# Performance work log

Hardware: AMD Instinct MI355X
Metric: run time of the kernel (lower is better)

The kernel has to match this reference:

```python
import jax, jax.numpy as jnp
import numpy as np

FH, FW = 3, 3          # kernel_size
SHIFT = 0.1            # input_shift


def extract_patches(x, fh, fw):
    # x: [B, C, H, W] -> patches flattened in (fh, fw, C) order: [B, fh*fw*C, Ho, Wo]
    B, C, H, W = x.shape
    Ho, Wo = H - fh + 1, W - fw + 1
    slices = [x[:, :, i:i + Ho, j:j + Wo] for i in range(fh) for j in range(fw)]
    p = jnp.stack(slices, axis=1)            # [B, fh*fw, C, Ho, Wo]
    return p.reshape(B, fh * fw * C, Ho, Wo)


def setup_inputs() -> dict:
    key = jax.random.key(0)
    kx, kk1, kk2 = jax.random.split(key, 3)
    B, C, H, W, O = 8, 32, 32, 32, 64
    x = jax.random.normal(kx, (B, C, H, W), dtype=jnp.float32)
    # xavier-uniform-style init for kernels (fh, fw, C, O)
    lim = float(np.sqrt(6.0 / (FH * FW * C + FH * FW * O)))
    k1 = jax.random.uniform(kk1, (FH, FW, C, O), minval=-lim, maxval=lim, dtype=jnp.float32)
    k2 = jax.random.uniform(kk2, (FH, FW, C, O), minval=-lim, maxval=lim, dtype=jnp.float32)
    bias = jnp.zeros((O,), dtype=jnp.float32)
    return {"x": x, "k1": k1, "k2": k2, "bias": bias}


def _branch(logp, kflat):
    # logp: [B, P, Ho, Wo], kflat: [P, O] -> max-plus over P, then exp: [B, O, Ho, Wo]
    return jnp.exp(jnp.max(logp[:, :, None, :, :] + kflat[None, :, :, None, None], axis=1))


def reference(x, k1, k2, bias):
    O = k1.shape[-1]
    k1f = k1.reshape(-1, O)   # (fh*fw*C, O) matches patch flatten order
    k2f = k2.reshape(-1, O)
    logp_pos = jnp.log(jnp.maximum(extract_patches(x, FH, FW), SHIFT))
    logp_neg = jnp.log(jnp.maximum(extract_patches(-x, FH, FW), SHIFT))
    y11 = _branch(logp_pos, k1f)
    y12 = _branch(logp_pos, k2f)
    y21 = _branch(logp_neg, k1f)
    y22 = _branch(logp_neg, k2f)
    return y11 - y12 - y21 + y22 + bias[None, :, None, None]
```

## Files before the change

### kernel.cpp

```cpp
#include <hip/hip_runtime.h>

namespace {

constexpr int FHc = 3, FWc = 3;
constexpr int Bc = 8, Cc = 32, Hc = 32, Wc = 32, Oc = 64;
constexpr int HOc = 30, WOc = 30;
constexpr float SHIFTc = 0.1f;
constexpr int SW = 4;
constexpr int RW = SW + FWc - 1;
constexpr int ROWW = 8;
constexpr int TILE_F = Cc * FHc * ROWW;

#define LOADROW6(dst, base) do {                                        \
    const float4 _a = *reinterpret_cast<const float4*>(base);           \
    const float2 _b = *reinterpret_cast<const float2*>((base) + 4);     \
    dst[0]=_a.x; dst[1]=_a.y; dst[2]=_a.z; dst[3]=_a.w;                 \
    dst[4]=_b.x; dst[5]=_b.y; } while (0)

__global__ __launch_bounds__(256, 4)
void bipolar_morph2d(const float* __restrict__ x,
                     const float* __restrict__ k1,
                     const float* __restrict__ k2,
                     const float* __restrict__ bias,
                     float* __restrict__ out)
{
    __shared__ float sh[4096];
    float* lp = sh;
    float* ln = sh + TILE_F;

    const int tid = threadIdx.x;
    const int bid = blockIdx.x;
    const int wt  = bid & 7;
    const int ho  = (bid >> 3) % HOc;
    const int b   = bid / (8 * HOc);
    const int wo0 = wt * SW;

    for (int e = tid; e < Cc * FHc * RW; e += 256) {
        const int c   = e / (FHc * RW);
        const int rem = e - c * (FHc * RW);
        const int i   = rem / RW;
        const int w   = rem - i * RW;
        int col = wo0 + w; if (col > Wc - 1) col = Wc - 1;
        const float xv = x[((b * Cc + c) * Hc + (ho + i)) * Wc + col];
        lp[(c * FHc + i) * ROWW + w] = __logf(fmaxf(xv,  SHIFTc));
        ln[(c * FHc + i) * ROWW + w] = __logf(fmaxf(-xv, SHIFTc));
    }
    __syncthreads();

    const int wv    = tid >> 6;
    const int o     = tid & 63;
    const int cbase = wv * 8;

    float m11[SW], m12[SW], m21[SW], m22[SW];
    #pragma unroll
    for (int s = 0; s < SW; ++s) m11[s] = m12[s] = m21[s] = m22[s] = -1e30f;

    #pragma unroll 1
    for (int c = cbase; c < cbase + 8; ++c) {
        #pragma unroll
        for (int i = 0; i < FHc; ++i) {
            const int p0 = (i * FWc * Cc + c) * Oc + o;
            const float k1j0 = k1[p0], k1j1 = k1[p0 + Cc * Oc], k1j2 = k1[p0 + 2 * Cc * Oc];
            const float k2j0 = k2[p0], k2j1 = k2[p0 + Cc * Oc], k2j2 = k2[p0 + 2 * Cc * Oc];

            float r[RW];
            LOADROW6(r, &lp[(c * FHc + i) * ROWW]);
            #pragma unroll
            for (int s = 0; s < SW; ++s) {
                m11[s] = fmaxf(m11[s], fmaxf(fmaxf(r[s] + k1j0, r[s + 1] + k1j1), r[s + 2] + k1j2));
                m12[s] = fmaxf(m12[s], fmaxf(fmaxf(r[s] + k2j0, r[s + 1] + k2j1), r[s + 2] + k2j2));
            }
            LOADROW6(r, &ln[(c * FHc + i) * ROWW]);
            #pragma unroll
            for (int s = 0; s < SW; ++s) {
                m21[s] = fmaxf(m21[s], fmaxf(fmaxf(r[s] + k1j0, r[s + 1] + k1j1), r[s + 2] + k1j2));
                m22[s] = fmaxf(m22[s], fmaxf(fmaxf(r[s] + k2j0, r[s + 1] + k2j1), r[s + 2] + k2j2));
            }
        }
    }

    __syncthreads();
    #pragma unroll
    for (int s = 0; s < SW; ++s) {
        sh[((wv * 4 + 0) * SW + s) * 64 + o] = m11[s];
        sh[((wv * 4 + 1) * SW + s) * 64 + o] = m12[s];
        sh[((wv * 4 + 2) * SW + s) * 64 + o] = m21[s];
        sh[((wv * 4 + 3) * SW + s) * 64 + o] = m22[s];
    }
    __syncthreads();

    const int s  = wv;
    const int wo = wo0 + s;
    if (wo < WOc) {
        const float bo = bias[o];
        float f[4];
        #pragma unroll
        for (int br = 0; br < 4; ++br) {
            const float v0 = sh[((0 * 4 + br) * SW + s) * 64 + o];
            const float v1 = sh[((1 * 4 + br) * SW + s) * 64 + o];
            const float v2 = sh[((2 * 4 + br) * SW + s) * 64 + o];
            const float v3 = sh[((3 * 4 + br) * SW + s) * 64 + o];
            f[br] = fmaxf(fmaxf(v0, v1), fmaxf(v2, v3));
        }
        out[((b * Oc + o) * HOc + ho) * WOc + wo] =
            __expf(f[0]) - __expf(f[1]) - __expf(f[2]) + __expf(f[3]) + bo;
    }
}

}

extern "C" void kernel_launch(void* const* d_in, const int* in_sizes, int n_in,
                              void* d_out, int out_size, void* d_ws, size_t ws_size,
                              hipStream_t stream) {
    const float* x    = (const float*)d_in[0];
    const float* k1   = (const float*)d_in[1];
    const float* k2   = (const float*)d_in[2];
    const float* bias = (const float*)d_in[3];
    float* out        = (float*)d_out;

    const int nblocks = Bc * HOc * 8;
    bipolar_morph2d<<<dim3(nblocks), dim3(256), 0, stream>>>(x, k1, k2, bias, out);
}
```

Measured before the change: 31.67 us.

## Precompute log-transformed input in prep kernel and read rows from global memory

Adds a prep kernel that computes log(max(±x, shift)) once for the whole input and interleaves k1/k2 into float2 pairs in the workspace. The main kernel then drops the per-block shared-memory staging and its barrier, and loads input rows straight from global/cache memory. Each loop iteration now handles two channels, which gives more independent max-plus work per step. The cost is a second kernel launch, a workspace round-trip, and reliance on cache hits for the repeated row loads.

Result: slower. 36.86 us (+16.4%).

```diff
diff --git a/kernel.cpp b/kernel.cpp
--- a/kernel.cpp
+++ b/kernel.cpp
@@ -7,26 +7,43 @@
 constexpr int HOc = 30, WOc = 30;
 constexpr float SHIFTc = 0.1f;
 constexpr int SW = 4;
-constexpr int RW = SW + FWc - 1;
-constexpr int ROWW = 8;
-constexpr int TILE_F = Cc * FHc * ROWW;
+constexpr int NX = Bc * Cc * Hc * Wc;
+constexpr int NK = FHc * FWc * Cc * Oc;
+constexpr int LN_OFF = NX;
+constexpr int KT_OFF = 2 * NX;
 
-#define LOADROW6(dst, base) do {                                        \
-    const float4 _a = *reinterpret_cast<const float4*>(base);           \
-    const float2 _b = *reinterpret_cast<const float2*>((base) + 4);     \
-    dst[0]=_a.x; dst[1]=_a.y; dst[2]=_a.z; dst[3]=_a.w;                 \
+__global__ __launch_bounds__(256)
+void prep_kernel(const float* __restrict__ x, const float* __restrict__ k1,
+                 const float* __restrict__ k2, float* __restrict__ ws)
+{
+    const int bid = blockIdx.x;
+    if (bid < NX / 256) {
+        const int t = bid * 256 + threadIdx.x;
+        const float xv = x[t];
+        ws[t]          = __logf(fmaxf(xv,  SHIFTc));
+        ws[LN_OFF + t] = __logf(fmaxf(-xv, SHIFTc));
+    } else {
+        const int t = (bid - NX / 256) * 256 + threadIdx.x;
+        if (t < NK) {
+            float2* kt = reinterpret_cast<float2*>(ws + KT_OFF);
+            kt[t] = make_float2(k1[t], k2[t]);
+        }
+    }
+}
+
+#define LDROW6(dst, p) do {                                              \
+    const float4 _a = *reinterpret_cast<const float4*>(p);               \
+    const float2 _b = *reinterpret_cast<const float2*>((p) + 4);         \
+    dst[0]=_a.x; dst[1]=_a.y; dst[2]=_a.z; dst[3]=_a.w;                  \
     dst[4]=_b.x; dst[5]=_b.y; } while (0)
 
+#define M3(m, a, b) (m) = fmaxf(fmaxf((m), (a)), (b))
+
 __global__ __launch_bounds__(256, 4)
-void bipolar_morph2d(const float* __restrict__ x,
-                     const float* __restrict__ k1,
-                     const float* __restrict__ k2,
-                     const float* __restrict__ bias,
-                     float* __restrict__ out)
+void bipolar_main(const float* __restrict__ ws, const float* __restrict__ bias,
+                  float* __restrict__ out)
 {
     __shared__ float sh[4096];
-    float* lp = sh;
-    float* ln = sh + TILE_F;
 
     const int tid = threadIdx.x;
     const int bid = blockIdx.x;
@@ -34,52 +51,54 @@
     const int ho  = (bid >> 3) % HOc;
     const int b   = bid / (8 * HOc);
     const int wo0 = wt * SW;
+    const int o   = tid & 63;
+    const int wv  = __builtin_amdgcn_readfirstlane(tid >> 6);
+    const int cbase = wv * 8;
 
-    for (int e = tid; e < Cc * FHc * RW; e += 256) {
-        const int c   = e / (FHc * RW);
-        const int rem = e - c * (FHc * RW);
-        const int i   = rem / RW;
-        const int w   = rem - i * RW;
-        int col = wo0 + w; if (col > Wc - 1) col = Wc - 1;
-        const float xv = x[((b * Cc + c) * Hc + (ho + i)) * Wc + col];
-        lp[(c * FHc + i) * ROWW + w] = __logf(fmaxf(xv,  SHIFTc));
-        ln[(c * FHc + i) * ROWW + w] = __logf(fmaxf(-xv, SHIFTc));
-    }
-    __syncthreads();
-
-    const int wv    = tid >> 6;
-    const int o     = tid & 63;
-    const int cbase = wv * 8;
+    const float2* __restrict__ kt = reinterpret_cast<const float2*>(ws + KT_OFF);
 
     float m11[SW], m12[SW], m21[SW], m22[SW];
     #pragma unroll
     for (int s = 0; s < SW; ++s) m11[s] = m12[s] = m21[s] = m22[s] = -1e30f;
 
     #pragma unroll 1
-    for (int c = cbase; c < cbase + 8; ++c) {
+    for (int cp = 0; cp < 4; ++cp) {
+        const int c0 = cbase + cp * 2;
         #pragma unroll
         for (int i = 0; i < FHc; ++i) {
-            const int p0 = (i * FWc * Cc + c) * Oc + o;
-            const float k1j0 = k1[p0], k1j1 = k1[p0 + Cc * Oc], k1j2 = k1[p0 + 2 * Cc * Oc];
-            const float k2j0 = k2[p0], k2j1 = k2[p0 + Cc * Oc], k2j2 = k2[p0 + 2 * Cc * Oc];
+            const float* lp0 = ws + ((b * Cc + c0) * Hc + (ho + i)) * Wc + wo0;
+            float rlp0[6], rlp1[6], rln0[6], rln1[6];
+            LDROW6(rlp0, lp0);
+            LDROW6(rlp1, lp0 + Hc * Wc);
+            LDROW6(rln0, lp0 + LN_OFF);
+            LDROW6(rln1, lp0 + LN_OFF + Hc * Wc);
 
-            float r[RW];
-            LOADROW6(r, &lp[(c * FHc + i) * ROWW]);
+            const int kb = (i * FWc * Cc + c0) * Oc + o;
+            const float2 ka0 = kt[kb],                 kb0 = kt[kb + Oc];
+            const float2 ka1 = kt[kb + Cc * Oc],       kb1 = kt[kb + Cc * Oc + Oc];
+            const float2 ka2 = kt[kb + 2 * Cc * Oc],   kb2 = kt[kb + 2 * Cc * Oc + Oc];
+
             #pragma unroll
             for (int s = 0; s < SW; ++s) {
-                m11[s] = fmaxf(m11[s], fmaxf(fmaxf(r[s] + k1j0, r[s + 1] + k1j1), r[s + 2] + k1j2));
-                m12[s] = fmaxf(m12[s], fmaxf(fmaxf(r[s] + k2j0, r[s + 1] + k2j1), r[s + 2] + k2j2));
-            }
-            LOADROW6(r, &ln[(c * FHc + i) * ROWW]);
-            #pragma unroll
-            for (int s = 0; s < SW; ++s) {
-                m21[s] = fmaxf(m21[s], fmaxf(fmaxf(r[s] + k1j0, r[s + 1] + k1j1), r[s + 2] + k1j2));
-                m22[s] = fmaxf(m22[s], fmaxf(fmaxf(r[s] + k2j0, r[s + 1] + k2j1), r[s + 2] + k2j2));
+                M3(m11[s], rlp0[s] + ka0.x, rlp0[s+1] + ka1.x);
+                M3(m11[s], rlp0[s+2] + ka2.x, rlp1[s] + kb0.x);
+                M3(m11[s], rlp1[s+1] + kb1.x, rlp1[s+2] + kb2.x);
+
+                M3(m12[s], rlp0[s] + ka0.y, rlp0[s+1] + ka1.y);
+                M3(m12[s], rlp0[s+2] + ka2.y, rlp1[s] + kb0.y);
+                M3(m12[s], rlp1[s+1] + kb1.y, rlp1[s+2] + kb2.y);
+
+                M3(m21[s], rln0[s] + ka0.x, rln0[s+1] + ka1.x);
+                M3(m21[s], rln0[s+2] + ka2.x, rln1[s] + kb0.x);
+                M3(m21[s], rln1[s+1] + kb1.x, rln1[s+2] + kb2.x);
+
+                M3(m22[s], rln0[s] + ka0.y, rln0[s+1] + ka1.y);
+                M3(m22[s], rln0[s+2] + ka2.y, rln1[s] + kb0.y);
+                M3(m22[s], rln1[s+1] + kb1.y, rln1[s+2] + kb2.y);
             }
         }
     }
 
-    __syncthreads();
     #pragma unroll
     for (int s = 0; s < SW; ++s) {
         sh[((wv * 4 + 0) * SW + s) * 64 + o] = m11[s];
@@ -116,8 +135,12 @@
     const float* k1   = (const float*)d_in[1];
     const float* k2   = (const float*)d_in[2];
     const float* bias = (const float*)d_in[3];
+    float* ws         = (float*)d_ws;
     float* out        = (float*)d_out;
 
-    const int nblocks = Bc * HOc * 8;
-    bipolar_morph2d<<<dim3(nblocks), dim3(256), 0, stream>>>(x, k1, k2, bias, out);
+    const int prep_blocks = NX / 256 + (NK + 255) / 256;
+    prep_kernel<<<dim3(prep_blocks), dim3(256), 0, stream>>>(x, k1, k2, ws);
+
+    const int main_blocks = Bc * HOc * 8;
+    bipolar_main<<<dim3(main_blocks), dim3(256), 0, stream>>>(ws, bias, out);
 }
```
